# Optimization experiments

Hardware: AMD Instinct MI355X
Metric: run time of the kernel (lower is better)

The kernel has to match this reference:

```python
import jax, jax.numpy as jnp
import numpy as np

N_HEAD = 12

def setup_inputs() -> dict:
    key = jax.random.key(0)
    ks = jax.random.split(key, 5)
    B, T, C = 8, 1024, 768
    s = 0.02
    return {
        'x': jax.random.normal(ks[0], (B, T, C), dtype=jnp.float32),
        'w_attn': jax.random.normal(ks[1], (C, 3 * C), dtype=jnp.float32) * s,
        'b_attn': jax.random.normal(ks[2], (3 * C,), dtype=jnp.float32) * s,
        'w_proj': jax.random.normal(ks[3], (C, C), dtype=jnp.float32) * s,
        'b_proj': jax.random.normal(ks[4], (C,), dtype=jnp.float32) * s,
    }

def reference(x, w_attn, b_attn, w_proj, b_proj):
    B, T, C = x.shape
    H, D = N_HEAD, C // N_HEAD
    qkv = x @ w_attn + b_attn                      # [B,T,3C]
    q, k, v = jnp.split(qkv, 3, axis=-1)
    q = q.reshape(B, T, H, D)
    k = k.reshape(B, T, H, D)
    v = v.reshape(B, T, H, D)
    # NOTE: faithful to source - NO 1/sqrt(D) scaling
    wei = jnp.einsum('bthd,bshd->bhts', q, k)      # [B,H,T,T]
    causal = jnp.tril(jnp.ones((T, T), dtype=bool))
    wei = jnp.where(causal[None, None], wei, -jnp.inf)
    wei = jax.nn.softmax(wei, axis=-1)
    out = jnp.einsum('bhts,bshd->bthd', wei, v)    # [B,T,H,D]
    out = out.reshape(B, T, C)
    return out @ w_proj + b_proj
```

## Files before the change

kernel.cpp:

```cpp
#include <hip/hip_runtime.h>

typedef __attribute__((ext_vector_type(8))) short bf16x8_t;
typedef __attribute__((ext_vector_type(4))) float f32x4_t;

#define AS1C(p) ((const __attribute__((address_space(1))) void*)(p))
#define AS3(p)  ((__attribute__((address_space(3))) void*)(p))

#define N_HEAD 12
#define SEQ_T 1024
#define CDIM 768
#define HDIM 64
#define L2E 1.44269504f

__device__ __forceinline__ unsigned short f2bf(float f) {
    union { float f; unsigned int u; } v;
    v.f = f;
    unsigned int r = (v.u + 0x7fffu + ((v.u >> 16) & 1u)) >> 16;
    return (unsigned short)r;
}

__global__ __launch_bounds__(256) void prep(
    const float4* __restrict__ x4, ushort4* __restrict__ xbf4,
    const float* __restrict__ w_attn, unsigned short* __restrict__ waT,
    const float* __restrict__ w_proj, unsigned short* __restrict__ wpT)
{
    __shared__ float tile[32][33];
    const int blk = blockIdx.x;
    const int tid = threadIdx.x;
    if (blk < 6144) {
        int i = blk * 256 + tid;
        float4 v = x4[i];
        ushort4 o;
        o.x = f2bf(v.x); o.y = f2bf(v.y); o.z = f2bf(v.z); o.w = f2bf(v.w);
        xbf4[i] = o;
        return;
    }
    const float* src; unsigned short* dst; int R, Cc, c0, r0;
    if (blk < 7872) {
        int idx = blk - 6144;
        src = w_attn; dst = waT; R = 768; Cc = 2304;
        c0 = (idx % 72) * 32; r0 = (idx / 72) * 32;
    } else {
        int idx = blk - 7872;
        src = w_proj; dst = wpT; R = 768; Cc = 768;
        c0 = (idx % 24) * 32; r0 = (idx / 24) * 32;
    }
    const int tx = tid & 31, ty = tid >> 5;
#pragma unroll
    for (int i = 0; i < 4; i++)
        tile[ty + i * 8][tx] = src[(size_t)(r0 + ty + i * 8) * Cc + c0 + tx];
    __syncthreads();
#pragma unroll
    for (int i = 0; i < 4; i++)
        dst[(size_t)(c0 + ty + i * 8) * R + r0 + tx] = f2bf(tile[tx][ty + i * 8]);
}

#define KTILES 12
#define ASTRIDE (128 * 64)
#define BSTRIDE (256 * 64)

__device__ __forceinline__ void stage_tile(
    const unsigned short* __restrict__ A, const unsigned short* __restrict__ Bt,
    unsigned short* As, unsigned short* Bs, int mBase, int nBase, int kt,
    int wv, int lane)
{
#pragma unroll
    for (int i = 0; i < 2; i++) {
        int cbase = i * 512 + wv * 64;
        int ci = cbase + lane;
        int r = ci >> 3;
        int koff = (((ci & 7) ^ (r & 7)) << 3);
        __builtin_amdgcn_global_load_lds(
            AS1C(A + (size_t)(mBase + r) * 768 + kt + koff),
            AS3(As + cbase * 8), 16, 0, 0);
    }
#pragma unroll
    for (int i = 0; i < 4; i++) {
        int cbase = i * 512 + wv * 64;
        int ci = cbase + lane;
        int r = ci >> 3;
        int koff = (((ci & 7) ^ (r & 7)) << 3);
        __builtin_amdgcn_global_load_lds(
            AS1C(Bt + (size_t)(nBase + r) * 768 + kt + koff),
            AS3(Bs + cbase * 8), 16, 0, 0);
    }
}

__device__ __forceinline__ void compute_tile(
    const unsigned short* As, const unsigned short* Bs,
    f32x4_t acc[4][4], int wm, int wn, int quad, int l16)
{
#pragma unroll
    for (int ks = 0; ks < 2; ks++) {
        bf16x8_t af[4], bfv[4];
#pragma unroll
        for (int tm = 0; tm < 4; tm++)
            af[tm] = *(const bf16x8_t*)(As + (wm + tm * 16 + l16) * 64 +
                                        (((ks * 4 + quad) ^ (l16 & 7)) << 3));
#pragma unroll
        for (int tn = 0; tn < 4; tn++)
            bfv[tn] = *(const bf16x8_t*)(Bs + (wn + tn * 16 + l16) * 64 +
                                         (((ks * 4 + quad) ^ (l16 & 7)) << 3));
#pragma unroll
        for (int tm = 0; tm < 4; tm++)
#pragma unroll
            for (int tn = 0; tn < 4; tn++)
                acc[tm][tn] = __builtin_amdgcn_mfma_f32_16x16x32_bf16(
                    af[tm], bfv[tn], acc[tm][tn], 0, 0, 0);
    }
}

__device__ __forceinline__ void gemm_core8(
    const unsigned short* __restrict__ A, const unsigned short* __restrict__ Bt,
    unsigned short* As, unsigned short* Bs, f32x4_t acc[4][4],
    int mBase, int nBase)
{
    const int tid  = threadIdx.x;
    const int lane = tid & 63;
    const int wv   = tid >> 6;
    const int quad = lane >> 4;
    const int l16  = lane & 15;
    const int wm   = (wv >> 2) * 64;
    const int wn   = (wv & 3) * 64;

    f32x4_t zero = {0.f, 0.f, 0.f, 0.f};
#pragma unroll
    for (int tm = 0; tm < 4; tm++)
#pragma unroll
        for (int tn = 0; tn < 4; tn++)
            acc[tm][tn] = zero;

    stage_tile(A, Bt, As + 0 * ASTRIDE, Bs + 0 * BSTRIDE, mBase, nBase, 0, wv, lane);
    stage_tile(A, Bt, As + 1 * ASTRIDE, Bs + 1 * BSTRIDE, mBase, nBase, 64, wv, lane);

#pragma unroll
    for (int t = 0; t < KTILES; t++) {
        if (t + 2 < KTILES) {
            const int nb = (t + 2) % 3;
            stage_tile(A, Bt, As + nb * ASTRIDE, Bs + nb * BSTRIDE,
                       mBase, nBase, (t + 2) * 64, wv, lane);
        }
        if (t + 2 < KTILES)
            asm volatile("s_waitcnt vmcnt(12)" ::: "memory");
        else if (t + 1 < KTILES)
            asm volatile("s_waitcnt vmcnt(6)" ::: "memory");
        else
            asm volatile("s_waitcnt vmcnt(0)" ::: "memory");
        __builtin_amdgcn_s_barrier();
        asm volatile("" ::: "memory");
        const int cb = t % 3;
        compute_tile(As + cb * ASTRIDE, Bs + cb * BSTRIDE, acc, wm, wn, quad, l16);
        asm volatile("" ::: "memory");
        __builtin_amdgcn_s_barrier();
    }
}

__global__ __launch_bounds__(512) void gemm_qkv(
    const unsigned short* __restrict__ x, const unsigned short* __restrict__ waT,
    const float* __restrict__ b_attn,
    unsigned short* __restrict__ qbuf, unsigned short* __restrict__ kbuf,
    unsigned short* __restrict__ vbuf)
{
    __shared__ __align__(16) unsigned short As[3 * ASTRIDE];
    __shared__ __align__(16) unsigned short Bs[3 * BSTRIDE];
    f32x4_t acc[4][4];
    const int lid = blockIdx.x;
    const int xcd = lid & 7;
    const int j = lid >> 3;
    const int mTile = xcd * 8 + (j & 7);
    const int nTile = j >> 3;
    const int mBase = mTile * 128;
    const int nBase = nTile * 256;
    gemm_core8(x, waT, As, Bs, acc, mBase, nBase);

    const int tid = threadIdx.x;
    const int lane = tid & 63, wv = tid >> 6;
    const int quad = lane >> 4, l16 = lane & 15;
    const int wm = (wv >> 2) * 64, wn = (wv & 3) * 64;
    const int part = nTile / 3;

#pragma unroll
    for (int tn = 0; tn < 4; tn++) {
        int n = nBase + wn + tn * 16 + l16;
        float bv = b_attn[n];
        int f = n - part * 768;
        int hh = f >> 6, d = f & 63;
        if (part == 2) {
#pragma unroll
            for (int tm = 0; tm < 4; tm++) {
                int t0 = mBase + wm + tm * 16 + quad * 4;
                int bb = t0 >> 10, tt = t0 & 1023;
                ushort4 pk;
                pk.x = f2bf(acc[tm][tn][0] + bv);
                pk.y = f2bf(acc[tm][tn][1] + bv);
                pk.z = f2bf(acc[tm][tn][2] + bv);
                pk.w = f2bf(acc[tm][tn][3] + bv);
                *(ushort4*)(vbuf + ((size_t)(bb * N_HEAD + hh) * HDIM + d) * SEQ_T + tt) = pk;
            }
        } else {
            const float scale = (part == 0) ? L2E : 1.f;
            unsigned short* dst = (part == 0) ? qbuf : kbuf;
#pragma unroll
            for (int tm = 0; tm < 4; tm++) {
#pragma unroll
                for (int i = 0; i < 4; i++) {
                    int row = mBase + wm + tm * 16 + quad * 4 + i;
                    int bb = row >> 10, tt = row & 1023;
                    dst[((size_t)(bb * N_HEAD + hh) * SEQ_T + tt) * HDIM + d] =
                        f2bf((acc[tm][tn][i] + bv) * scale);
                }
            }
        }
    }
}

__device__ __forceinline__ void mask_exp_pack(
    f32x4_t s[4], int diag, int qloc, int quad,
    float& lsum, unsigned int u[4][2])
{
    if (diag) {
#pragma unroll
        for (int c = 0; c < 4; c++)
#pragma unroll
            for (int i = 0; i < 4; i++)
                if (c * 16 + quad * 4 + i > qloc) s[c][i] = -1e30f;
    }
    float p[4][4];
#pragma unroll
    for (int c = 0; c < 4; c++)
#pragma unroll
        for (int i = 0; i < 4; i++)
            p[c][i] = exp2f(s[c][i]);
#pragma unroll
    for (int c = 0; c < 4; c++)
        lsum += (p[c][0] + p[c][1]) + (p[c][2] + p[c][3]);
#pragma unroll
    for (int c = 0; c < 4; c++)
#pragma unroll
        for (int i2 = 0; i2 < 2; i2++)
            u[c][i2] = (unsigned int)f2bf(p[c][2 * i2]) |
                       ((unsigned int)f2bf(p[c][2 * i2 + 1]) << 16);
}

__device__ __forceinline__ void p_write(
    unsigned short* pw, const unsigned int u[4][2], int quad, int l16)
{
#pragma unroll
    for (int c = 0; c < 4; c++)
#pragma unroll
        for (int i2 = 0; i2 < 2; i2++) {
            int g = c * 2 + (quad >> 1);
            *(unsigned int*)(pw + l16 * 64 + ((g ^ (l16 & 7)) << 3) +
                             4 * (quad & 1) + 2 * i2) = u[c][i2];
        }
}

__global__ __launch_bounds__(256, 3) void attn_fused(
    const unsigned short* __restrict__ qb, const unsigned short* __restrict__ kb,
    const unsigned short* __restrict__ vb, unsigned short* __restrict__ attb)
{
    __shared__ __align__(16) unsigned short Kbuf[2][64 * 64];
    __shared__ __align__(16) unsigned short Vbuf[2][64 * 64];
    __shared__ __align__(16) unsigned short Psh[4][16 * 64];

    const int bhx = blockIdx.x;
    const int t   = blockIdx.y;
    const int h = bhx % N_HEAD;
    const int b = bhx / N_HEAD;
    const int tid = threadIdx.x;
    const int lane = tid & 63, wv = tid >> 6;
    const int quad = lane >> 4, l16 = lane & 15;
    const int tB = 15 - t, kmax = 15 - t;
    const int qloc = wv * 16 + l16;

    const size_t bh = (size_t)(b * N_HEAD + h);
    const unsigned short* kbase = kb + bh * SEQ_T * HDIM;
    const unsigned short* vbase = vb + bh * HDIM * SEQ_T;
    const unsigned short* qpt   = qb + bh * SEQ_T * HDIM;

    const int j0 = wv * 128 + lane, j1 = j0 + 64;
    const int r0 = j0 >> 3, g0 = (j0 & 7) ^ (r0 & 7);
    const int r1 = j1 >> 3, g1 = (j1 & 7) ^ (r1 & 7);
    const int rgK0 = r0 * 64 + g0 * 8,   rgK1 = r1 * 64 + g1 * 8;
    const int rgV0 = r0 * 1024 + g0 * 8, rgV1 = r1 * 1024 + g1 * 8;
    const int ldsc0 = (wv * 128) * 8, ldsc1 = (wv * 128 + 64) * 8;

    bf16x8_t qfA[2], qfB[2];
    {
        const unsigned short* qa  = qpt + (size_t)(t * 64 + qloc) * HDIM;
        const unsigned short* qbp = qpt + (size_t)(tB * 64 + qloc) * HDIM;
#pragma unroll
        for (int kc = 0; kc < 2; kc++) {
            qfA[kc] = *(const bf16x8_t*)(qa + kc * 32 + quad * 8);
            qfB[kc] = *(const bf16x8_t*)(qbp + kc * 32 + quad * 8);
        }
    }

    f32x4_t zero = {0.f, 0.f, 0.f, 0.f};
    f32x4_t oA[4], oB[4];
#pragma unroll
    for (int c = 0; c < 4; c++) { oA[c] = zero; oB[c] = zero; }
    float lA = 0.f, lB = 0.f;

    __builtin_amdgcn_global_load_lds(AS1C(kbase + rgK0), AS3(&Kbuf[0][0] + ldsc0), 16, 0, 0);
    __builtin_amdgcn_global_load_lds(AS1C(kbase + rgK1), AS3(&Kbuf[0][0] + ldsc1), 16, 0, 0);
    __builtin_amdgcn_global_load_lds(AS1C(vbase + rgV0), AS3(&Vbuf[0][0] + ldsc0), 16, 0, 0);
    __builtin_amdgcn_global_load_lds(AS1C(vbase + rgV1), AS3(&Vbuf[0][0] + ldsc1), 16, 0, 0);
    __syncthreads();

    for (int kt = 0; kt <= kmax; kt++) {
        const int cur = kt & 1, nxt = cur ^ 1;
        if (kt < kmax) {
            const unsigned short* kp = kbase + (kt + 1) * 4096;
            const unsigned short* vp = vbase + (kt + 1) * 64;
            __builtin_amdgcn_global_load_lds(AS1C(kp + rgK0), AS3(&Kbuf[nxt][0] + ldsc0), 16, 0, 0);
            __builtin_amdgcn_global_load_lds(AS1C(kp + rgK1), AS3(&Kbuf[nxt][0] + ldsc1), 16, 0, 0);
            __builtin_amdgcn_global_load_lds(AS1C(vp + rgV0), AS3(&Vbuf[nxt][0] + ldsc0), 16, 0, 0);
            __builtin_amdgcn_global_load_lds(AS1C(vp + rgV1), AS3(&Vbuf[nxt][0] + ldsc1), 16, 0, 0);
        }

        const unsigned short* Kc = &Kbuf[cur][0];
        const unsigned short* Vc = &Vbuf[cur][0];
        const int doA = (kt <= t);

        bf16x8_t vf[4][2];
#pragma unroll
        for (int nc = 0; nc < 4; nc++)
#pragma unroll
            for (int kc = 0; kc < 2; kc++)
                vf[nc][kc] = *(const bf16x8_t*)(Vc + (nc * 16 + l16) * 64 +
                                                (((kc * 4 + quad) ^ (l16 & 7)) << 3));

        f32x4_t sB[4], sA[4];
#pragma unroll
        for (int c = 0; c < 4; c++) {
            bf16x8_t kf0 = *(const bf16x8_t*)(Kc + (c * 16 + l16) * 64 +
                                              ((quad ^ (l16 & 7)) << 3));
            bf16x8_t kf1 = *(const bf16x8_t*)(Kc + (c * 16 + l16) * 64 +
                                              (((4 + quad) ^ (l16 & 7)) << 3));
            sB[c] = __builtin_amdgcn_mfma_f32_16x16x32_bf16(kf0, qfB[0], zero, 0, 0, 0);
            sB[c] = __builtin_amdgcn_mfma_f32_16x16x32_bf16(kf1, qfB[1], sB[c], 0, 0, 0);
            if (doA) {
                sA[c] = __builtin_amdgcn_mfma_f32_16x16x32_bf16(kf0, qfA[0], zero, 0, 0, 0);
                sA[c] = __builtin_amdgcn_mfma_f32_16x16x32_bf16(kf1, qfA[1], sA[c], 0, 0, 0);
            }
        }

        unsigned short* pw = &Psh[wv][0];
        unsigned int uB[4][2], uA[4][2];

        mask_exp_pack(sB, kt == tB, qloc, quad, lB, uB);
        __asm__ __volatile__("" ::: "memory");
        p_write(pw, uB, quad, l16);
        if (doA)
            mask_exp_pack(sA, kt == t, qloc, quad, lA, uA);
        __asm__ __volatile__("" ::: "memory");
        bf16x8_t pfB[2];
#pragma unroll
        for (int kc = 0; kc < 2; kc++)
            pfB[kc] = *(const bf16x8_t*)(pw + l16 * 64 + (((kc * 4 + quad) ^ (l16 & 7)) << 3));
        __asm__ __volatile__("" ::: "memory");
#pragma unroll
        for (int kc = 0; kc < 2; kc++)
#pragma unroll
            for (int nc = 0; nc < 4; nc++)
                oB[nc] = __builtin_amdgcn_mfma_f32_16x16x32_bf16(pfB[kc], vf[nc][kc], oB[nc], 0, 0, 0);
        if (doA) {
            p_write(pw, uA, quad, l16);
            __asm__ __volatile__("" ::: "memory");
            bf16x8_t pfA[2];
#pragma unroll
            for (int kc = 0; kc < 2; kc++)
                pfA[kc] = *(const bf16x8_t*)(pw + l16 * 64 + (((kc * 4 + quad) ^ (l16 & 7)) << 3));
#pragma unroll
            for (int kc = 0; kc < 2; kc++)
#pragma unroll
                for (int nc = 0; nc < 4; nc++)
                    oA[nc] = __builtin_amdgcn_mfma_f32_16x16x32_bf16(pfA[kc], vf[nc][kc], oA[nc], 0, 0, 0);
        }
        __syncthreads();
    }

    lA += __shfl_xor(lA, 16); lA += __shfl_xor(lA, 32);
    lB += __shfl_xor(lB, 16); lB += __shfl_xor(lB, 32);
    float invA = 1.f / lA, invB = 1.f / lB;
    float iA[4], iB[4];
#pragma unroll
    for (int i = 0; i < 4; i++) {
        iA[i] = __shfl(invA, quad * 4 + i);
        iB[i] = __shfl(invB, quad * 4 + i);
    }

#pragma unroll
    for (int nc = 0; nc < 4; nc++)
#pragma unroll
        for (int i = 0; i < 4; i++) {
            int rowA = t * 64 + wv * 16 + quad * 4 + i;
            int rowB = tB * 64 + wv * 16 + quad * 4 + i;
            int col = h * HDIM + nc * 16 + l16;
            attb[((size_t)b * SEQ_T + rowA) * CDIM + col] = f2bf(oA[nc][i] * iA[i]);
            attb[((size_t)b * SEQ_T + rowB) * CDIM + col] = f2bf(oB[nc][i] * iB[i]);
        }
}

__global__ __launch_bounds__(512) void gemm_proj(
    const unsigned short* __restrict__ attb, const unsigned short* __restrict__ wpT,
    const float* __restrict__ b_proj, float* __restrict__ out)
{
    __shared__ __align__(16) unsigned short As[3 * ASTRIDE];
    __shared__ __align__(16) unsigned short Bs[3 * BSTRIDE];
    f32x4_t acc[4][4];
    const int lid = blockIdx.x;
    const int xcd = lid & 7;
    const int j = lid >> 3;
    const int mTile = xcd * 8 + (j & 7);
    const int nTile = j >> 3;
    const int mBase = mTile * 128;
    const int nBase = nTile * 256;
    gemm_core8(attb, wpT, As, Bs, acc, mBase, nBase);

    const int tid  = threadIdx.x;
    const int lane = tid & 63;
    const int wv   = tid >> 6;
    const int quad = lane >> 4;
    const int l16  = lane & 15;
    const int wm   = (wv >> 2) * 64;
    const int wn   = (wv & 3) * 64;

#pragma unroll
    for (int tn = 0; tn < 4; tn++) {
        int n = nBase + wn + tn * 16 + l16;
        float bv = b_proj[n];
#pragma unroll
        for (int tm = 0; tm < 4; tm++)
#pragma unroll
            for (int i = 0; i < 4; i++) {
                int row = mBase + wm + tm * 16 + quad * 4 + i;
                out[(size_t)row * CDIM + n] = acc[tm][tn][i] + bv;
            }
    }
}

extern "C" void kernel_launch(void* const* d_in, const int* in_sizes, int n_in,
                              void* d_out, int out_size, void* d_ws, size_t ws_size,
                              hipStream_t stream) {
    const float* x      = (const float*)d_in[0];
    const float* w_attn = (const float*)d_in[1];
    const float* b_attn = (const float*)d_in[2];
    const float* w_proj = (const float*)d_in[3];
    const float* b_proj = (const float*)d_in[4];
    float* out = (float*)d_out;

    unsigned short* ws   = (unsigned short*)d_ws;
    unsigned short* waT  = ws;
    unsigned short* wpT  = waT + 1769472;
    unsigned short* xbf  = wpT + 589824;
    unsigned short* qbuf = xbf + 6291456;
    unsigned short* kbuf = qbuf + 6291456;
    unsigned short* vbuf = kbuf + 6291456;
    unsigned short* attb = vbuf + 6291456;

    prep<<<dim3(8448), 256, 0, stream>>>((const float4*)x, (ushort4*)xbf,
                                         w_attn, waT, w_proj, wpT);
    gemm_qkv<<<dim3(576), 512, 0, stream>>>(xbf, waT, b_attn, qbuf, kbuf, vbuf);
    attn_fused<<<dim3(96, 8), 256, 0, stream>>>(qbuf, kbuf, vbuf, attb);
    gemm_proj<<<dim3(192), 512, 0, stream>>>(attb, wpT, b_proj, out);
}
```

Baseline: 182.3 us.

## Switch QKV and proj GEMMs to 256x256 tiles with 8-phase pipelined schedule

```diff
diff --git a/kernel.cpp b/kernel.cpp
--- a/kernel.cpp
+++ b/kernel.cpp
@@ -55,128 +55,172 @@
         dst[(size_t)(c0 + ty + i * 8) * R + r0 + tx] = f2bf(tile[tx][ty + i * 8]);
 }
 
-#define KTILES 12
-#define ASTRIDE (128 * 64)
-#define BSTRIDE (256 * 64)
-
-__device__ __forceinline__ void stage_tile(
-    const unsigned short* __restrict__ A, const unsigned short* __restrict__ Bt,
-    unsigned short* As, unsigned short* Bs, int mBase, int nBase, int kt,
-    int wv, int lane)
+__device__ __forceinline__ void stage_half(
+    const unsigned short* __restrict__ src, int rowBase, int kt,
+    unsigned short* lds_half, int wv, int lane)
 {
 #pragma unroll
     for (int i = 0; i < 2; i++) {
         int cbase = i * 512 + wv * 64;
         int ci = cbase + lane;
         int r = ci >> 3;
-        int koff = (((ci & 7) ^ (r & 7)) << 3);
+        int gk = (ci & 7) ^ (r & 7);
         __builtin_amdgcn_global_load_lds(
-            AS1C(A + (size_t)(mBase + r) * 768 + kt + koff),
-            AS3(As + cbase * 8), 16, 0, 0);
-    }
-#pragma unroll
-    for (int i = 0; i < 4; i++) {
-        int cbase = i * 512 + wv * 64;
-        int ci = cbase + lane;
-        int r = ci >> 3;
-        int koff = (((ci & 7) ^ (r & 7)) << 3);
-        __builtin_amdgcn_global_load_lds(
-            AS1C(Bt + (size_t)(nBase + r) * 768 + kt + koff),
-            AS3(Bs + cbase * 8), 16, 0, 0);
-    }
-}
-
-__device__ __forceinline__ void compute_tile(
-    const unsigned short* As, const unsigned short* Bs,
-    f32x4_t acc[4][4], int wm, int wn, int quad, int l16)
-{
-#pragma unroll
-    for (int ks = 0; ks < 2; ks++) {
-        bf16x8_t af[4], bfv[4];
-#pragma unroll
-        for (int tm = 0; tm < 4; tm++)
-            af[tm] = *(const bf16x8_t*)(As + (wm + tm * 16 + l16) * 64 +
-                                        (((ks * 4 + quad) ^ (l16 & 7)) << 3));
-#pragma unroll
-        for (int tn = 0; tn < 4; tn++)
-            bfv[tn] = *(const bf16x8_t*)(Bs + (wn + tn * 16 + l16) * 64 +
-                                         (((ks * 4 + quad) ^ (l16 & 7)) << 3));
-#pragma unroll
-        for (int tm = 0; tm < 4; tm++)
-#pragma unroll
-            for (int tn = 0; tn < 4; tn++)
-                acc[tm][tn] = __builtin_amdgcn_mfma_f32_16x16x32_bf16(
-                    af[tm], bfv[tn], acc[tm][tn], 0, 0, 0);
-    }
-}
-
-__device__ __forceinline__ void gemm_core8(
-    const unsigned short* __restrict__ A, const unsigned short* __restrict__ Bt,
-    unsigned short* As, unsigned short* Bs, f32x4_t acc[4][4],
-    int mBase, int nBase)
-{
+            AS1C(src + (size_t)(rowBase + r) * 768 + kt + gk * 8),
+            AS3(lds_half + cbase * 8), 16, 0, 0);
+    }
+}
+
+__device__ __forceinline__ void gemm256_8phase(
+    const unsigned short* __restrict__ Ag, const unsigned short* __restrict__ Bg,
+    f32x4_t acc[8][4], int mBase, int nBase)
+{
+    __shared__ __align__(16) unsigned short As[2][2][128 * 64];
+    __shared__ __align__(16) unsigned short Bs[2][2][128 * 64];
+
     const int tid  = threadIdx.x;
     const int lane = tid & 63;
     const int wv   = tid >> 6;
     const int quad = lane >> 4;
     const int l16  = lane & 15;
-    const int wm   = (wv >> 2) * 64;
-    const int wn   = (wv & 3) * 64;
+    const int wr   = wv >> 2;
+    const int wc   = wv & 3;
+    const int brow = (wc & 1) * 64;
 
     f32x4_t zero = {0.f, 0.f, 0.f, 0.f};
 #pragma unroll
-    for (int tm = 0; tm < 4; tm++)
-#pragma unroll
-        for (int tn = 0; tn < 4; tn++)
-            acc[tm][tn] = zero;
-
-    stage_tile(A, Bt, As + 0 * ASTRIDE, Bs + 0 * BSTRIDE, mBase, nBase, 0, wv, lane);
-    stage_tile(A, Bt, As + 1 * ASTRIDE, Bs + 1 * BSTRIDE, mBase, nBase, 64, wv, lane);
-
-#pragma unroll
-    for (int t = 0; t < KTILES; t++) {
-        if (t + 2 < KTILES) {
-            const int nb = (t + 2) % 3;
-            stage_tile(A, Bt, As + nb * ASTRIDE, Bs + nb * BSTRIDE,
-                       mBase, nBase, (t + 2) * 64, wv, lane);
-        }
-        if (t + 2 < KTILES)
-            asm volatile("s_waitcnt vmcnt(12)" ::: "memory");
-        else if (t + 1 < KTILES)
-            asm volatile("s_waitcnt vmcnt(6)" ::: "memory");
-        else
-            asm volatile("s_waitcnt vmcnt(0)" ::: "memory");
-        __builtin_amdgcn_s_barrier();
-        asm volatile("" ::: "memory");
-        const int cb = t % 3;
-        compute_tile(As + cb * ASTRIDE, Bs + cb * BSTRIDE, acc, wm, wn, quad, l16);
-        asm volatile("" ::: "memory");
-        __builtin_amdgcn_s_barrier();
-    }
-}
-
-__global__ __launch_bounds__(512) void gemm_qkv(
+    for (int m = 0; m < 8; m++)
+#pragma unroll
+        for (int n = 0; n < 4; n++)
+            acc[m][n] = zero;
+
+    stage_half(Ag, mBase,       0,  &As[0][0][0], wv, lane);
+    stage_half(Ag, mBase + 128, 0,  &As[0][1][0], wv, lane);
+    stage_half(Bg, nBase,       0,  &Bs[0][0][0], wv, lane);
+    stage_half(Bg, nBase + 128, 0,  &Bs[0][1][0], wv, lane);
+    stage_half(Ag, mBase,       64, &As[1][0][0], wv, lane);
+    asm volatile("s_waitcnt vmcnt(2)" ::: "memory");
+    __builtin_amdgcn_s_barrier();
+    asm volatile("" ::: "memory");
+
+#define RD_A(dst, tmv, kkv)                                                    \
+    dst = *(const bf16x8_t*)(Acur + ((tmv) * 16 + l16) * 64 +                  \
+                             ((((kkv) * 4 + quad) ^ (l16 & 7)) << 3))
+#define RD_B(dst, tnv, kkv)                                                    \
+    dst = *(const bf16x8_t*)(Bcur + (brow + (tnv) * 16 + l16) * 64 +           \
+                             ((((kkv) * 4 + quad) ^ (l16 & 7)) << 3))
+#define STAGE_G(g)                                                             \
+    {                                                                          \
+        const int s_ = (g) + 5;                                                \
+        const int js0 = s_ >> 2;                                               \
+        const int js = (js0 >= 12) ? js0 - 2 : js0;    \
+        const int hh = s_ & 3;                                                 \
+        const int kts = js * 64;                                               \
+        if (hh == 0)      stage_half(Ag, mBase,       kts, &As[js & 1][0][0], wv, lane); \
+        else if (hh == 1) stage_half(Ag, mBase + 128, kts, &As[js & 1][1][0], wv, lane); \
+        else if (hh == 2) stage_half(Bg, nBase,       kts, &Bs[js & 1][0][0], wv, lane); \
+        else              stage_half(Bg, nBase + 128, kts, &Bs[js & 1][1][0], wv, lane); \
+    }
+#define BAR_PRE()                                                              \
+    asm volatile("" ::: "memory");                                             \
+    __builtin_amdgcn_s_barrier();                                              \
+    asm volatile("" ::: "memory");                                             \
+    __builtin_amdgcn_s_setprio(1);
+#define BAR_POST(q)                                                            \
+    __builtin_amdgcn_s_setprio(0);                                             \
+    if ((q) == 3) asm volatile("s_waitcnt vmcnt(2)" ::: "memory");             \
+    asm volatile("" ::: "memory");                                             \
+    __builtin_amdgcn_s_barrier();                                              \
+    asm volatile("" ::: "memory");
+#define MM(m, n, a, b2)                                                        \
+    acc[m][n] = __builtin_amdgcn_mfma_f32_16x16x32_bf16(a, b2, acc[m][n], 0, 0, 0)
+
+#pragma unroll
+    for (int jj = 0; jj < 12; ++jj) {
+        const unsigned short* Acur = &As[jj & 1][wr][0];
+        const unsigned short* Bcur = &Bs[jj & 1][wc >> 1][0];
+        bf16x8_t a03[4][2], a47[4][2], b01[2][2], b23[2][2];
+
+#pragma unroll
+        for (int m = 0; m < 4; m++) { RD_A(a03[m][0], m, 0); RD_A(a03[m][1], m, 1); }
+#pragma unroll
+        for (int n = 0; n < 2; n++) { RD_B(b01[n][0], n, 0); RD_B(b01[n][1], n, 1); }
+        STAGE_G(jj * 4 + 0);
+        BAR_PRE();
+#pragma unroll
+        for (int k = 0; k < 2; k++)
+#pragma unroll
+            for (int m = 0; m < 4; m++)
+#pragma unroll
+                for (int n = 0; n < 2; n++)
+                    MM(m, n, a03[m][k], b01[n][k]);
+        BAR_POST(0);
+
+#pragma unroll
+        for (int n = 0; n < 2; n++) { RD_B(b23[n][0], 2 + n, 0); RD_B(b23[n][1], 2 + n, 1); }
+        STAGE_G(jj * 4 + 1);
+        BAR_PRE();
+#pragma unroll
+        for (int k = 0; k < 2; k++)
+#pragma unroll
+            for (int m = 0; m < 4; m++)
+#pragma unroll
+                for (int n = 0; n < 2; n++)
+                    MM(m, 2 + n, a03[m][k], b23[n][k]);
+        BAR_POST(1);
+
+#pragma unroll
+        for (int m = 0; m < 4; m++) { RD_A(a47[m][0], 4 + m, 0); RD_A(a47[m][1], 4 + m, 1); }
+        STAGE_G(jj * 4 + 2);
+        BAR_PRE();
+#pragma unroll
+        for (int k = 0; k < 2; k++)
+#pragma unroll
+            for (int m = 0; m < 4; m++)
+#pragma unroll
+                for (int n = 0; n < 2; n++)
+                    MM(4 + m, n, a47[m][k], b01[n][k]);
+        BAR_POST(2);
+
+        STAGE_G(jj * 4 + 3);
+        BAR_PRE();
+#pragma unroll
+        for (int k = 0; k < 2; k++)
+#pragma unroll
+            for (int m = 0; m < 4; m++)
+#pragma unroll
+                for (int n = 0; n < 2; n++)
+                    MM(4 + m, 2 + n, a47[m][k], b23[n][k]);
+        BAR_POST(3);
+    }
+#undef RD_A
+#undef RD_B
+#undef STAGE_G
+#undef BAR_PRE
+#undef BAR_POST
+#undef MM
+}
+
+__global__ __launch_bounds__(512, 2) void gemm_qkv(
     const unsigned short* __restrict__ x, const unsigned short* __restrict__ waT,
     const float* __restrict__ b_attn,
     unsigned short* __restrict__ qbuf, unsigned short* __restrict__ kbuf,
     unsigned short* __restrict__ vbuf)
 {
-    __shared__ __align__(16) unsigned short As[3 * ASTRIDE];
-    __shared__ __align__(16) unsigned short Bs[3 * BSTRIDE];
-    f32x4_t acc[4][4];
+    f32x4_t acc[8][4];
     const int lid = blockIdx.x;
     const int xcd = lid & 7;
     const int j = lid >> 3;
-    const int mTile = xcd * 8 + (j & 7);
-    const int nTile = j >> 3;
-    const int mBase = mTile * 128;
+    const int mTile = xcd * 4 + (j & 3);
+    const int nTile = j >> 2;
+    const int mBase = mTile * 256;
     const int nBase = nTile * 256;
-    gemm_core8(x, waT, As, Bs, acc, mBase, nBase);
+    gemm256_8phase(x, waT, acc, mBase, nBase);
 
     const int tid = threadIdx.x;
     const int lane = tid & 63, wv = tid >> 6;
     const int quad = lane >> 4, l16 = lane & 15;
-    const int wm = (wv >> 2) * 64, wn = (wv & 3) * 64;
+    const int wm = (wv >> 2) * 128, wn = (wv & 3) * 64;
     const int part = nTile / 3;
 
 #pragma unroll
@@ -187,7 +231,7 @@
         int hh = f >> 6, d = f & 63;
         if (part == 2) {
 #pragma unroll
-            for (int tm = 0; tm < 4; tm++) {
+            for (int tm = 0; tm < 8; tm++) {
                 int t0 = mBase + wm + tm * 16 + quad * 4;
                 int bb = t0 >> 10, tt = t0 & 1023;
                 ushort4 pk;
@@ -201,7 +245,7 @@
             const float scale = (part == 0) ? L2E : 1.f;
             unsigned short* dst = (part == 0) ? qbuf : kbuf;
 #pragma unroll
-            for (int tm = 0; tm < 4; tm++) {
+            for (int tm = 0; tm < 8; tm++) {
 #pragma unroll
                 for (int i = 0; i < 4; i++) {
                     int row = mBase + wm + tm * 16 + quad * 4 + i;
@@ -403,28 +447,26 @@
         }
 }
 
-__global__ __launch_bounds__(512) void gemm_proj(
+__global__ __launch_bounds__(512, 2) void gemm_proj(
     const unsigned short* __restrict__ attb, const unsigned short* __restrict__ wpT,
     const float* __restrict__ b_proj, float* __restrict__ out)
 {
-    __shared__ __align__(16) unsigned short As[3 * ASTRIDE];
-    __shared__ __align__(16) unsigned short Bs[3 * BSTRIDE];
-    f32x4_t acc[4][4];
+    f32x4_t acc[8][4];
     const int lid = blockIdx.x;
     const int xcd = lid & 7;
     const int j = lid >> 3;
-    const int mTile = xcd * 8 + (j & 7);
-    const int nTile = j >> 3;
-    const int mBase = mTile * 128;
+    const int mTile = xcd * 4 + (j & 3);
+    const int nTile = j >> 2;
+    const int mBase = mTile * 256;
     const int nBase = nTile * 256;
-    gemm_core8(attb, wpT, As, Bs, acc, mBase, nBase);
+    gemm256_8phase(attb, wpT, acc, mBase, nBase);
 
     const int tid  = threadIdx.x;
     const int lane = tid & 63;
     const int wv   = tid >> 6;
     const int quad = lane >> 4;
     const int l16  = lane & 15;
-    const int wm   = (wv >> 2) * 64;
+    const int wm   = (wv >> 2) * 128;
     const int wn   = (wv & 3) * 64;
 
 #pragma unroll
@@ -432,7 +474,7 @@
         int n = nBase + wn + tn * 16 + l16;
         float bv = b_proj[n];
 #pragma unroll
-        for (int tm = 0; tm < 4; tm++)
+        for (int tm = 0; tm < 8; tm++)
 #pragma unroll
             for (int i = 0; i < 4; i++) {
                 int row = mBase + wm + tm * 16 + quad * 4 + i;
@@ -462,7 +504,7 @@
 
     prep<<<dim3(8448), 256, 0, stream>>>((const float4*)x, (ushort4*)xbf,
                                          w_attn, waT, w_proj, wpT);
-    gemm_qkv<<<dim3(576), 512, 0, stream>>>(xbf, waT, b_attn, qbuf, kbuf, vbuf);
+    gemm_qkv<<<dim3(288), 512, 0, stream>>>(xbf, waT, b_attn, qbuf, kbuf, vbuf);
     attn_fused<<<dim3(96, 8), 256, 0, stream>>>(qbuf, kbuf, vbuf, attb);
-    gemm_proj<<<dim3(192), 512, 0, stream>>>(attb, wpT, b_proj, out);
-}
+    gemm_proj<<<dim3(96), 512, 0, stream>>>(attb, wpT, b_proj, out);
+}
```

After: 200.3 us. 1.1x slower.

## Switch QKV GEMM to 128x128 tiles with 256 threads and double buffering

Applied to the files above, without the earlier changes.

```diff
diff --git a/kernel.cpp b/kernel.cpp
--- a/kernel.cpp
+++ b/kernel.cpp
@@ -55,73 +55,38 @@
         dst[(size_t)(c0 + ty + i * 8) * R + r0 + tx] = f2bf(tile[tx][ty + i * 8]);
 }
 
-#define KTILES 12
-#define ASTRIDE (128 * 64)
-#define BSTRIDE (256 * 64)
-
-__device__ __forceinline__ void stage_tile(
+__device__ __forceinline__ void stage128(
     const unsigned short* __restrict__ A, const unsigned short* __restrict__ Bt,
     unsigned short* As, unsigned short* Bs, int mBase, int nBase, int kt,
     int wv, int lane)
 {
 #pragma unroll
-    for (int i = 0; i < 2; i++) {
-        int cbase = i * 512 + wv * 64;
+    for (int i = 0; i < 4; i++) {
+        int cbase = i * 256 + wv * 64;
         int ci = cbase + lane;
         int r = ci >> 3;
         int koff = (((ci & 7) ^ (r & 7)) << 3);
         __builtin_amdgcn_global_load_lds(
             AS1C(A + (size_t)(mBase + r) * 768 + kt + koff),
             AS3(As + cbase * 8), 16, 0, 0);
-    }
-#pragma unroll
-    for (int i = 0; i < 4; i++) {
-        int cbase = i * 512 + wv * 64;
-        int ci = cbase + lane;
-        int r = ci >> 3;
-        int koff = (((ci & 7) ^ (r & 7)) << 3);
         __builtin_amdgcn_global_load_lds(
             AS1C(Bt + (size_t)(nBase + r) * 768 + kt + koff),
             AS3(Bs + cbase * 8), 16, 0, 0);
     }
 }
 
-__device__ __forceinline__ void compute_tile(
-    const unsigned short* As, const unsigned short* Bs,
-    f32x4_t acc[4][4], int wm, int wn, int quad, int l16)
-{
-#pragma unroll
-    for (int ks = 0; ks < 2; ks++) {
-        bf16x8_t af[4], bfv[4];
-#pragma unroll
-        for (int tm = 0; tm < 4; tm++)
-            af[tm] = *(const bf16x8_t*)(As + (wm + tm * 16 + l16) * 64 +
-                                        (((ks * 4 + quad) ^ (l16 & 7)) << 3));
-#pragma unroll
-        for (int tn = 0; tn < 4; tn++)
-            bfv[tn] = *(const bf16x8_t*)(Bs + (wn + tn * 16 + l16) * 64 +
-                                         (((ks * 4 + quad) ^ (l16 & 7)) << 3));
-#pragma unroll
-        for (int tm = 0; tm < 4; tm++)
-#pragma unroll
-            for (int tn = 0; tn < 4; tn++)
-                acc[tm][tn] = __builtin_amdgcn_mfma_f32_16x16x32_bf16(
-                    af[tm], bfv[tn], acc[tm][tn], 0, 0, 0);
-    }
-}
-
-__device__ __forceinline__ void gemm_core8(
+__device__ __forceinline__ void gemm128_core(
     const unsigned short* __restrict__ A, const unsigned short* __restrict__ Bt,
-    unsigned short* As, unsigned short* Bs, f32x4_t acc[4][4],
-    int mBase, int nBase)
+    unsigned short (*As)[128 * 64], unsigned short (*Bs)[128 * 64],
+    f32x4_t acc[4][4], int mBase, int nBase)
 {
     const int tid  = threadIdx.x;
     const int lane = tid & 63;
     const int wv   = tid >> 6;
     const int quad = lane >> 4;
     const int l16  = lane & 15;
-    const int wm   = (wv >> 2) * 64;
-    const int wn   = (wv & 3) * 64;
+    const int wm   = (wv >> 1) * 64;
+    const int wn   = (wv & 1) * 64;
 
     f32x4_t zero = {0.f, 0.f, 0.f, 0.f};
 #pragma unroll
@@ -130,39 +95,47 @@
         for (int tn = 0; tn < 4; tn++)
             acc[tm][tn] = zero;
 
-    stage_tile(A, Bt, As + 0 * ASTRIDE, Bs + 0 * BSTRIDE, mBase, nBase, 0, wv, lane);
-    stage_tile(A, Bt, As + 1 * ASTRIDE, Bs + 1 * BSTRIDE, mBase, nBase, 64, wv, lane);
-
-#pragma unroll
-    for (int t = 0; t < KTILES; t++) {
-        if (t + 2 < KTILES) {
-            const int nb = (t + 2) % 3;
-            stage_tile(A, Bt, As + nb * ASTRIDE, Bs + nb * BSTRIDE,
-                       mBase, nBase, (t + 2) * 64, wv, lane);
-        }
-        if (t + 2 < KTILES)
-            asm volatile("s_waitcnt vmcnt(12)" ::: "memory");
-        else if (t + 1 < KTILES)
-            asm volatile("s_waitcnt vmcnt(6)" ::: "memory");
-        else
-            asm volatile("s_waitcnt vmcnt(0)" ::: "memory");
-        __builtin_amdgcn_s_barrier();
-        asm volatile("" ::: "memory");
-        const int cb = t % 3;
-        compute_tile(As + cb * ASTRIDE, Bs + cb * BSTRIDE, acc, wm, wn, quad, l16);
-        asm volatile("" ::: "memory");
-        __builtin_amdgcn_s_barrier();
-    }
-}
-
-__global__ __launch_bounds__(512) void gemm_qkv(
+    stage128(A, Bt, As[0], Bs[0], mBase, nBase, 0, wv, lane);
+    __syncthreads();
+
+    for (int kt = 0; kt < 12; kt++) {
+        const int cur = kt & 1;
+        if (kt < 11)
+            stage128(A, Bt, As[cur ^ 1], Bs[cur ^ 1], mBase, nBase,
+                     (kt + 1) * 64, wv, lane);
+        __asm__ __volatile__("" ::: "memory");
+        const unsigned short* Ac = As[cur];
+        const unsigned short* Bc = Bs[cur];
+#pragma unroll
+        for (int ks = 0; ks < 2; ks++) {
+            bf16x8_t af[4], bfv[4];
+#pragma unroll
+            for (int tm = 0; tm < 4; tm++)
+                af[tm] = *(const bf16x8_t*)(Ac + (wm + tm * 16 + l16) * 64 +
+                                            (((ks * 4 + quad) ^ (l16 & 7)) << 3));
+#pragma unroll
+            for (int tn = 0; tn < 4; tn++)
+                bfv[tn] = *(const bf16x8_t*)(Bc + (wn + tn * 16 + l16) * 64 +
+                                             (((ks * 4 + quad) ^ (l16 & 7)) << 3));
+#pragma unroll
+            for (int tm = 0; tm < 4; tm++)
+#pragma unroll
+                for (int tn = 0; tn < 4; tn++)
+                    acc[tm][tn] = __builtin_amdgcn_mfma_f32_16x16x32_bf16(
+                        af[tm], bfv[tn], acc[tm][tn], 0, 0, 0);
+        }
+        __syncthreads();
+    }
+}
+
+__global__ __launch_bounds__(256) void gemm_qkv(
     const unsigned short* __restrict__ x, const unsigned short* __restrict__ waT,
     const float* __restrict__ b_attn,
     unsigned short* __restrict__ qbuf, unsigned short* __restrict__ kbuf,
     unsigned short* __restrict__ vbuf)
 {
-    __shared__ __align__(16) unsigned short As[3 * ASTRIDE];
-    __shared__ __align__(16) unsigned short Bs[3 * BSTRIDE];
+    __shared__ __align__(16) unsigned short As[2][128 * 64];
+    __shared__ __align__(16) unsigned short Bs[2][128 * 64];
     f32x4_t acc[4][4];
     const int lid = blockIdx.x;
     const int xcd = lid & 7;
@@ -170,14 +143,14 @@
     const int mTile = xcd * 8 + (j & 7);
     const int nTile = j >> 3;
     const int mBase = mTile * 128;
-    const int nBase = nTile * 256;
-    gemm_core8(x, waT, As, Bs, acc, mBase, nBase);
+    const int nBase = nTile * 128;
+    gemm128_core(x, waT, As, Bs, acc, mBase, nBase);
 
     const int tid = threadIdx.x;
     const int lane = tid & 63, wv = tid >> 6;
     const int quad = lane >> 4, l16 = lane & 15;
-    const int wm = (wv >> 2) * 64, wn = (wv & 3) * 64;
-    const int part = nTile / 3;
+    const int wm = (wv >> 1) * 64, wn = (wv & 1) * 64;
+    const int part = nTile / 6;
 
 #pragma unroll
     for (int tn = 0; tn < 4; tn++) {
@@ -214,6 +187,106 @@
     }
 }
 
+#define KTILES 12
+#define ASTRIDE (128 * 64)
+#define BSTRIDE (256 * 64)
+
+__device__ __forceinline__ void stage_tile(
+    const unsigned short* __restrict__ A, const unsigned short* __restrict__ Bt,
+    unsigned short* As, unsigned short* Bs, int mBase, int nBase, int kt,
+    int wv, int lane)
+{
+#pragma unroll
+    for (int i = 0; i < 2; i++) {
+        int cbase = i * 512 + wv * 64;
+        int ci = cbase + lane;
+        int r = ci >> 3;
+        int koff = (((ci & 7) ^ (r & 7)) << 3);
+        __builtin_amdgcn_global_load_lds(
+            AS1C(A + (size_t)(mBase + r) * 768 + kt + koff),
+            AS3(As + cbase * 8), 16, 0, 0);
+    }
+#pragma unroll
+    for (int i = 0; i < 4; i++) {
+        int cbase = i * 512 + wv * 64;
+        int ci = cbase + lane;
+        int r = ci >> 3;
+        int koff = (((ci & 7) ^ (r & 7)) << 3);
+        __builtin_amdgcn_global_load_lds(
+            AS1C(Bt + (size_t)(nBase + r) * 768 + kt + koff),
+            AS3(Bs + cbase * 8), 16, 0, 0);
+    }
+}
+
+__device__ __forceinline__ void compute_tile(
+    const unsigned short* As, const unsigned short* Bs,
+    f32x4_t acc[4][4], int wm, int wn, int quad, int l16)
+{
+#pragma unroll
+    for (int ks = 0; ks < 2; ks++) {
+        bf16x8_t af[4], bfv[4];
+#pragma unroll
+        for (int tm = 0; tm < 4; tm++)
+            af[tm] = *(const bf16x8_t*)(As + (wm + tm * 16 + l16) * 64 +
+                                        (((ks * 4 + quad) ^ (l16 & 7)) << 3));
+#pragma unroll
+        for (int tn = 0; tn < 4; tn++)
+            bfv[tn] = *(const bf16x8_t*)(Bs + (wn + tn * 16 + l16) * 64 +
+                                         (((ks * 4 + quad) ^ (l16 & 7)) << 3));
+#pragma unroll
+        for (int tm = 0; tm < 4; tm++)
+#pragma unroll
+            for (int tn = 0; tn < 4; tn++)
+                acc[tm][tn] = __builtin_amdgcn_mfma_f32_16x16x32_bf16(
+                    af[tm], bfv[tn], acc[tm][tn], 0, 0, 0);
+    }
+}
+
+__device__ __forceinline__ void gemm_core8(
+    const unsigned short* __restrict__ A, const unsigned short* __restrict__ Bt,
+    unsigned short* As, unsigned short* Bs, f32x4_t acc[4][4],
+    int mBase, int nBase)
+{
+    const int tid  = threadIdx.x;
+    const int lane = tid & 63;
+    const int wv   = tid >> 6;
+    const int quad = lane >> 4;
+    const int l16  = lane & 15;
+    const int wm   = (wv >> 2) * 64;
+    const int wn   = (wv & 3) * 64;
+
+    f32x4_t zero = {0.f, 0.f, 0.f, 0.f};
+#pragma unroll
+    for (int tm = 0; tm < 4; tm++)
+#pragma unroll
+        for (int tn = 0; tn < 4; tn++)
+            acc[tm][tn] = zero;
+
+    stage_tile(A, Bt, As + 0 * ASTRIDE, Bs + 0 * BSTRIDE, mBase, nBase, 0, wv, lane);
+    stage_tile(A, Bt, As + 1 * ASTRIDE, Bs + 1 * BSTRIDE, mBase, nBase, 64, wv, lane);
+
+#pragma unroll
+    for (int t = 0; t < KTILES; t++) {
+        if (t + 2 < KTILES) {
+            const int nb = (t + 2) % 3;
+            stage_tile(A, Bt, As + nb * ASTRIDE, Bs + nb * BSTRIDE,
+                       mBase, nBase, (t + 2) * 64, wv, lane);
+        }
+        if (t + 2 < KTILES)
+            asm volatile("s_waitcnt vmcnt(12)" ::: "memory");
+        else if (t + 1 < KTILES)
+            asm volatile("s_waitcnt vmcnt(6)" ::: "memory");
+        else
+            asm volatile("s_waitcnt vmcnt(0)" ::: "memory");
+        __builtin_amdgcn_s_barrier();
+        asm volatile("" ::: "memory");
+        const int cb = t % 3;
+        compute_tile(As + cb * ASTRIDE, Bs + cb * BSTRIDE, acc, wm, wn, quad, l16);
+        asm volatile("" ::: "memory");
+        __builtin_amdgcn_s_barrier();
+    }
+}
+
 __device__ __forceinline__ void mask_exp_pack(
     f32x4_t s[4], int diag, int qloc, int quad,
     float& lsum, unsigned int u[4][2])
@@ -462,7 +535,7 @@
 
     prep<<<dim3(8448), 256, 0, stream>>>((const float4*)x, (ushort4*)xbf,
                                          w_attn, waT, w_proj, wpT);
-    gemm_qkv<<<dim3(576), 512, 0, stream>>>(xbf, waT, b_attn, qbuf, kbuf, vbuf);
+    gemm_qkv<<<dim3(1152), 256, 0, stream>>>(xbf, waT, b_attn, qbuf, kbuf, vbuf);
     attn_fused<<<dim3(96, 8), 256, 0, stream>>>(qbuf, kbuf, vbuf, attb);
     gemm_proj<<<dim3(192), 512, 0, stream>>>(attb, wpT, b_proj, out);
 }
```

New measurement: 181.6 us. Within noise of the previous version (-0.4%).
